# Optimization experiments

Hardware: AMD Instinct MI355X
Metric: run time of the kernel (lower is better)

Reference implementation:

```python
import jax, jax.numpy as jnp
import numpy as np

B, S, E, H, FF = 4, 2048, 512, 8, 2048
DH = E // H
EPS = 1e-6


def setup_inputs() -> dict:
    key = jax.random.key(0)
    ks = jax.random.split(key, 16)
    sc = lambda fan_in: 1.0 / np.sqrt(fan_in)
    inp = {
        "x": jax.random.normal(ks[0], (B, S, E), dtype=jnp.float32),
        "src_mask": jnp.ones((B, 1, 1, S), dtype=jnp.int32),
        # attention projections, stored [in, out]
        "wq": jax.random.uniform(ks[1], (E, E), minval=-sc(E), maxval=sc(E)),
        "bq": jnp.zeros((E,), jnp.float32),
        "wk": jax.random.uniform(ks[2], (E, E), minval=-sc(E), maxval=sc(E)),
        "bk": jnp.zeros((E,), jnp.float32),
        "wv": jax.random.uniform(ks[3], (E, E), minval=-sc(E), maxval=sc(E)),
        "bv": jnp.zeros((E,), jnp.float32),
        "wo": jax.random.uniform(ks[4], (E, E), minval=-sc(E), maxval=sc(E)),
        "bo": jnp.zeros((E,), jnp.float32),
        # feed-forward
        "w1": jax.random.uniform(ks[5], (E, FF), minval=-sc(E), maxval=sc(E)),
        "b1": jnp.zeros((FF,), jnp.float32),
        "w2": jax.random.uniform(ks[6], (FF, E), minval=-sc(FF), maxval=sc(FF)),
        "b2": jnp.zeros((E,), jnp.float32),
        # addNormLayer scalar params (alpha init 1, bias init 0)
        "alpha1": jnp.ones((1,), jnp.float32),
        "beta1": jnp.zeros((1,), jnp.float32),
        "alpha2": jnp.ones((1,), jnp.float32),
        "beta2": jnp.zeros((1,), jnp.float32),
    }
    return inp


def _norm(x, alpha, beta):
    # matches torch: mean + unbiased std (ddof=1), eps added to std
    mean = jnp.mean(x, axis=-1, keepdims=True)
    std = jnp.std(x, axis=-1, keepdims=True, ddof=1)
    return alpha * (x - mean) / (std + EPS) + beta


def reference(x, src_mask, wq, bq, wk, bk, wv, bv, wo, bo,
              w1, b1, w2, b2, alpha1, beta1, alpha2, beta2):
    # --- residual 1: pre-norm self-attention ---
    n = _norm(x, alpha1, beta1)  # [B,S,E]
    q = (n @ wq + bq).reshape(B, S, H, DH).transpose(0, 2, 1, 3)  # [B,H,S,DH]
    k = (n @ wk + bk).reshape(B, S, H, DH).transpose(0, 2, 1, 3)
    v = (n @ wv + bv).reshape(B, S, H, DH).transpose(0, 2, 1, 3)
    scores = jnp.einsum('bhqd,bhkd->bhqk', q, k) / np.sqrt(DH)  # [B,H,S,S]
    scores = jnp.where(src_mask == 0, -1e9, scores)
    attn = jax.nn.softmax(scores, axis=-1)
    ctx = jnp.einsum('bhqk,bhkd->bhqd', attn, v)  # [B,H,S,DH]
    ctx = ctx.transpose(0, 2, 1, 3).reshape(B, S, E)
    x = x + (ctx @ wo + bo)
    # --- residual 2: pre-norm FFN ---
    n2 = _norm(x, alpha2, beta2)
    ff = jax.nn.relu(n2 @ w1 + b1) @ w2 + b2
    return x + ff
```

## Files before the change

### kernel.cpp

```cpp
#include <hip/hip_runtime.h>

typedef __bf16 bfrag __attribute__((ext_vector_type(8)));
typedef float f32x4 __attribute__((ext_vector_type(4)));
typedef float f32x16 __attribute__((ext_vector_type(16)));
typedef unsigned short us8 __attribute__((ext_vector_type(8)));
typedef unsigned int u32x2 __attribute__((ext_vector_type(2)));
typedef unsigned int u32x4 __attribute__((ext_vector_type(4)));

__device__ __forceinline__ float bf2f(unsigned short s) {
  unsigned u = ((unsigned)s) << 16;
  float f;
  __builtin_memcpy(&f, &u, 4);
  return f;
}
__device__ __forceinline__ unsigned short f2bf(float f) {
  unsigned u;
  __builtin_memcpy(&u, &f, 4);
  u += 0x7fffu + ((u >> 16) & 1u);
  return (unsigned short)(u >> 16);
}
__device__ __forceinline__ float rdf(const void* p, size_t i, int isf) {
  return isf ? ((const float*)p)[i] : bf2f(((const unsigned short*)p)[i]);
}
__device__ __forceinline__ void gld16(const unsigned short* g, unsigned short* l) {
  __builtin_amdgcn_global_load_lds(
      (const __attribute__((address_space(1))) unsigned int*)g,
      (__attribute__((address_space(3))) unsigned int*)l, 16, 0, 0);
}
__device__ __forceinline__ unsigned cvtpk_bf16(float a, float b) {
  unsigned d;
  asm("v_cvt_pk_bf16_f32 %0, %1, %2" : "=v"(d) : "v"(a), "v"(b));
  return d;
}

template <int XMODE>
__device__ void norm_unit(const void* xin, const void* alpha, const void* beta,
                          unsigned short* out, int isf, int u) {
  constexpr int E = 512;
  int xf = XMODE ? 1 : isf;
  int tid = threadIdx.x;
  int wave = tid >> 6, lane = tid & 63;
  size_t tok = (size_t)u * 4 + wave;
  float v[8];
  if (xf) {
    const float* xp = (const float*)xin + tok * E + lane * 8;
    float4 a0 = *(const float4*)xp;
    float4 a1 = *(const float4*)(xp + 4);
    v[0] = a0.x; v[1] = a0.y; v[2] = a0.z; v[3] = a0.w;
    v[4] = a1.x; v[5] = a1.y; v[6] = a1.z; v[7] = a1.w;
  } else {
    us8 uu = *(const us8*)((const unsigned short*)xin + tok * E + lane * 8);
#pragma unroll
    for (int j = 0; j < 8; j++) v[j] = bf2f(uu[j]);
  }
  float s = 0.f, sq = 0.f;
#pragma unroll
  for (int j = 0; j < 8; j++) { s += v[j]; sq += v[j] * v[j]; }
#pragma unroll
  for (int off = 1; off < 64; off <<= 1) {
    s += __shfl_xor(s, off, 64);
    sq += __shfl_xor(sq, off, 64);
  }
  float mean = s * (1.0f / 512.0f);
  float var = fmaxf((sq - 512.0f * mean * mean) * (1.0f / 511.0f), 0.0f);
  float inv = rdf(alpha, 0, isf) / (sqrtf(var) + 1e-6f);
  float be = rdf(beta, 0, isf);
  us8 ov;
#pragma unroll
  for (int j = 0; j < 8; j++) ov[j] = f2bf((v[j] - mean) * inv + be);
  *(us8*)(out + tok * E + lane * 8) = ov;
}

__global__ __launch_bounds__(256) void setup_k(
    const unsigned short* __restrict__ x16,
    const void* wq, const void* wk, const void* wv, const void* wo,
    const void* w1, const void* w2,
    unsigned short* wqkvT, unsigned short* woT,
    unsigned short* w1T, unsigned short* w2T,
    const void* bq, const void* bk, const void* bv, const void* bo,
    const void* b1, const void* b2, float* __restrict__ bcat,
    const void* alpha1, const void* beta1, unsigned short* __restrict__ n1,
    int* __restrict__ flag) {
  __shared__ unsigned short tile[32][33];
  __shared__ int s_cnt;
  int tid = threadIdx.x;
  int bid = blockIdx.x;
  if (tid == 0) s_cnt = 0;
  __syncthreads();
  {
    int c = 0;
    for (int i = tid; i < 4096; i += 256) {
      unsigned short s = x16[2 * i];
      int e = (s >> 7) & 0xFF;
      if (e > 0xC2 || (e != 0 && e < 0x3D)) c++;
    }
    atomicAdd(&s_cnt, c);
  }
  __syncthreads();
  const int isf = (s_cnt > 256) ? 1 : 0;
  if (bid == 0 && tid == 0) flag[0] = isf;

  if (bid >= 3090) {
    norm_unit<0>(x16, alpha1, beta1, n1, isf, bid - 3090);
    return;
  }
  if (bid >= 3072) {
    int i = (bid - 3072) * 256 + tid;
    if (i < 4608) {
      float v;
      if (i < 512) v = rdf(bq, i, isf);
      else if (i < 1024) v = rdf(bk, i - 512, isf);
      else if (i < 1536) v = rdf(bv, i - 1024, isf);
      else if (i < 2048) v = rdf(bo, i - 1536, isf);
      else if (i < 4096) v = rdf(b1, i - 2048, isf);
      else v = rdf(b2, i - 4096, isf);
      bcat[i] = v;
    }
    return;
  }
  const void* W;
  unsigned short* Wt;
  int K, N, t;
  if (bid < 1024) {
    K = 512; N = 512; t = bid & 255;
    if (bid < 256) { W = wq; Wt = wqkvT; }
    else if (bid < 512) { W = wk; Wt = wqkvT + 262144; }
    else if (bid < 768) { W = wv; Wt = wqkvT + 524288; }
    else { W = wo; Wt = woT; }
  } else if (bid < 2048) {
    W = w1; Wt = w1T; K = 512; N = 2048; t = bid - 1024;
  } else {
    W = w2; Wt = w2T; K = 2048; N = 512; t = bid - 2048;
  }
  int nx = N >> 5;
  int n0 = (t % nx) * 32, k0 = (t / nx) * 32;
#pragma unroll
  for (int i = 0; i < 4; i++) {
    int e = tid + i * 256;
    int r = e >> 5, c = e & 31;
    tile[r][c] = f2bf(rdf(W, (size_t)(k0 + r) * N + n0 + c, isf));
  }
  __syncthreads();
#pragma unroll
  for (int i = 0; i < 4; i++) {
    int e = tid + i * 256;
    int r = e >> 5, c = e & 31;
    Wt[(size_t)(n0 + r) * K + k0 + c] = tile[c][r];
  }
}

__global__ __launch_bounds__(256) void vtrans_k(
    const unsigned short* __restrict__ qkb, unsigned short* __restrict__ vbt) {
  __shared__ unsigned short tile[32][33];
  int tid = threadIdx.x;
  int u = blockIdx.x;
  int s0 = (u & 63) * 32;
  int d0 = ((u >> 6) & 1) * 32;
  int bh = u >> 7, b = bh >> 3, h = bh & 7;
#pragma unroll
  for (int i = 0; i < 4; i++) {
    int e = tid + i * 256;
    int r = e >> 5, c = e & 31;
    tile[r][c] = qkb[((size_t)b * 2048 + s0 + r) * 1536 + 1024 + h * 64 + d0 + c];
  }
  __syncthreads();
#pragma unroll
  for (int i = 0; i < 4; i++) {
    int e = tid + i * 256;
    int r = e >> 5, c = e & 31;
    vbt[((size_t)bh * 64 + d0 + r) * 2048 + s0 + c] = tile[c][r];
  }
}

__global__ __launch_bounds__(256) void norm2_k(
    const void* __restrict__ xin, const void* __restrict__ alpha,
    const void* __restrict__ beta, unsigned short* __restrict__ out,
    const int* __restrict__ flag) {
  norm_unit<1>(xin, alpha, beta, out, flag[0], blockIdx.x);
}

template <int TN, int RES, int OUTM, int RELU>
__global__ __launch_bounds__(256, 3) void gemm2_k(
    const unsigned short* __restrict__ A,
    const unsigned short* __restrict__ Bt,
    const float* __restrict__ bias,
    const void* __restrict__ res,
    void* __restrict__ outp,
    int N, int K, const int* __restrict__ flag) {
  constexpr int MT = (TN == 128) ? 4 : 2;
  constexpr int BROWS = TN / 4;
  __shared__ alignas(16) unsigned short As[128 * 64];
  __shared__ alignas(16) unsigned short Bs[TN * 64];
  int isf = flag[0];
  int outf32 = (OUTM == 1) || (OUTM == 2 && isf);
  int tid = threadIdx.x;
  int wave = tid >> 6, lane = tid & 63;
  int quad = lane >> 4, l16 = lane & 15, l7 = l16 & 7;
  int wm = (TN == 128) ? (wave >> 1) : wave;
  int wn = (TN == 128) ? (wave & 1) : 0;
  size_t m0 = (size_t)blockIdx.x * 128;
  size_t n0 = (size_t)blockIdx.y * TN;

  int lrow = lane >> 3;
  int gcol = 8 * ((lane & 7) ^ lrow);

  const unsigned short* ag = A + (m0 + wave * 32 + lrow) * K + gcol;
  const unsigned short* bg = Bt + (n0 + wave * BROWS + lrow) * K + gcol;
  unsigned short* asl = &As[(wave * 32) * 64];
  unsigned short* bsl = &Bs[(wave * BROWS) * 64];

  f32x4 acc[MT][4];
#pragma unroll
  for (int i = 0; i < MT; i++)
#pragma unroll
    for (int j = 0; j < 4; j++) acc[i][j] = {0.f, 0.f, 0.f, 0.f};

  for (int k0 = 0; k0 < K; k0 += 64) {
    __syncthreads();
#pragma unroll
    for (int c = 0; c < 4; c++)
      gld16(ag + (size_t)(8 * c) * K + k0, asl + (8 * c) * 64);
#pragma unroll
    for (int c = 0; c < BROWS / 8; c++)
      gld16(bg + (size_t)(8 * c) * K + k0, bsl + (8 * c) * 64);
    __syncthreads();
#pragma unroll
    for (int ko = 0; ko < 2; ko++) {
      int slot = ((4 * ko + quad) ^ l7) * 8;
      bfrag af[MT], bf[4];
#pragma unroll
      for (int i = 0; i < MT; i++)
        af[i] = *(const bfrag*)&As[(wm * (MT * 16) + i * 16 + l16) * 64 + slot];
#pragma unroll
      for (int j = 0; j < 4; j++)
        bf[j] = *(const bfrag*)&Bs[(wn * 64 + j * 16 + l16) * 64 + slot];
#pragma unroll
      for (int i = 0; i < MT; i++)
#pragma unroll
        for (int j = 0; j < 4; j++)
          acc[i][j] = __builtin_amdgcn_mfma_f32_16x16x32_bf16(af[i], bf[j], acc[i][j], 0, 0, 0);
    }
  }
#pragma unroll
  for (int j = 0; j < 4; j++) {
    size_t n = n0 + wn * 64 + j * 16 + l16;
    float bv = bias[n];
#pragma unroll
    for (int i = 0; i < MT; i++) {
#pragma unroll
      for (int r = 0; r < 4; r++) {
        size_t m = m0 + wm * (MT * 16) + i * 16 + quad * 4 + r;
        float vv = acc[i][j][r] + bv;
        if (RELU) vv = fmaxf(vv, 0.0f);
        if (RES == 1) vv += rdf(res, m * N + n, isf);
        else if (RES == 2) vv += ((const float*)res)[m * N + n];
        if (outf32) ((float*)outp)[m * N + n] = vv;
        else ((unsigned short*)outp)[m * N + n] = f2bf(vv);
      }
    }
  }
}

__global__ __launch_bounds__(256, 2) void attn_k(
    const unsigned short* __restrict__ qkb,
    const unsigned short* __restrict__ vbt,
    const int* __restrict__ mask,
    unsigned short* __restrict__ ctx) {
  constexpr int S = 2048;
  __shared__ alignas(16) unsigned short Kt[64 * 64];
  __shared__ alignas(16) unsigned short Vt[64 * 64];
  __shared__ alignas(16) float mskf[64];
  __shared__ float linv[128];
  int tid = threadIdx.x, wave = tid >> 6, lane = tid & 63;
  int l32 = lane & 31, hi = lane >> 5;
  int q0 = blockIdx.x * 128;
  int bh = blockIdx.y, b = bh >> 3, h = bh & 7;
  size_t rowbase = (size_t)b * S;
  const float SC = 0.18033688f;

  bfrag qf[4];
  {
    const unsigned short* qp =
        qkb + (rowbase + q0 + wave * 32 + l32) * 1536 + h * 64 + hi * 8;
#pragma unroll
    for (int ds = 0; ds < 4; ds++) qf[ds] = *(const bfrag*)(qp + ds * 16);
  }

  int srow_l = lane >> 3;
  int sc = lane & 7;
  const unsigned short* kgb = qkb + 512 + h * 64;
  const unsigned short* vgb = vbt + (size_t)bh * 64 * S;

  f32x16 o[2];
#pragma unroll
  for (int i = 0; i < 16; i++) { o[0][i] = 0.f; o[1][i] = 0.f; }
  float l_i = 0.f;

  for (int kt = 0; kt < S; kt += 64) {
    __syncthreads();
    {
#pragma unroll
      for (int i = 0; i < 2; i++) {
        int r = wave * 16 + i * 8 + srow_l;
        gld16(kgb + (rowbase + kt + r) * 1536 + (size_t)((sc ^ (r & 7)) * 8),
              &Kt[(wave * 16 + i * 8) * 64]);
        gld16(vgb + (size_t)r * S + kt + (size_t)((sc ^ (r & 7)) * 8),
              &Vt[(wave * 16 + i * 8) * 64]);
      }
    }
    if (tid < 64) mskf[tid] = mask[rowbase + kt + tid] ? 0.0f : -1e5f;
    __syncthreads();

    f32x16 pacc[2];
#pragma unroll
    for (int t = 0; t < 2; t++)
#pragma unroll
      for (int i = 0; i < 16; i++) pacc[t][i] = 0.f;
#pragma unroll
    for (int t = 0; t < 2; t++) {
      int r = t * 32 + l32;
#pragma unroll
      for (int ds = 0; ds < 4; ds++) {
        int phys = ((2 * ds + hi) ^ (r & 7)) * 8;
        bfrag kf = *(const bfrag*)&Kt[r * 64 + phys];
        pacc[t] = __builtin_amdgcn_mfma_f32_32x32x16_bf16(kf, qf[ds], pacc[t], 0, 0, 0);
      }
    }

    unsigned pb[2][8];
#pragma unroll
    for (int t = 0; t < 2; t++) {
#pragma unroll
      for (int g = 0; g < 4; g++) {
        float4 m4 = *(const float4*)&mskf[t * 32 + g * 8 + hi * 4];
        float p0 = __builtin_amdgcn_exp2f(fminf(fmaf(pacc[t][g * 4 + 0], SC, m4.x), 50.0f));
        float p1 = __builtin_amdgcn_exp2f(fminf(fmaf(pacc[t][g * 4 + 1], SC, m4.y), 50.0f));
        float p2 = __builtin_amdgcn_exp2f(fminf(fmaf(pacc[t][g * 4 + 2], SC, m4.z), 50.0f));
        float p3 = __builtin_amdgcn_exp2f(fminf(fmaf(pacc[t][g * 4 + 3], SC, m4.w), 50.0f));
        l_i += (p0 + p1) + (p2 + p3);
        pb[t][g * 2] = cvtpk_bf16(p0, p1);
        pb[t][g * 2 + 1] = cvtpk_bf16(p2, p3);
      }
    }

#pragma unroll
    for (int ks = 0; ks < 4; ks++) {
      int t = ks >> 1, e = ks & 1;
      u32x2 sA = __builtin_amdgcn_permlane32_swap(pb[t][4 * e + 0], pb[t][4 * e + 2], false, false);
      u32x2 sB = __builtin_amdgcn_permlane32_swap(pb[t][4 * e + 1], pb[t][4 * e + 3], false, false);
      u32x4 pw = {sA.x, sB.x, sA.y, sB.y};
      bfrag pf = __builtin_bit_cast(bfrag, pw);
#pragma unroll
      for (int dt = 0; dt < 2; dt++) {
        int r = dt * 32 + l32;
        int phys = ((2 * ks + hi) ^ (r & 7)) * 8;
        bfrag vf = *(const bfrag*)&Vt[r * 64 + phys];
        o[dt] = __builtin_amdgcn_mfma_f32_32x32x16_bf16(pf, vf, o[dt], 0, 0, 0);
      }
    }
  }

  {
    unsigned lu = __builtin_bit_cast(unsigned, l_i);
    u32x2 lr = __builtin_amdgcn_permlane32_swap(lu, lu, false, false);
    float l_tot = __builtin_bit_cast(float, lr.x) + __builtin_bit_cast(float, lr.y);
    if (lane < 32) linv[wave * 32 + l32] = 1.0f / fmaxf(l_tot, 1e-30f);
  }
  __syncthreads();
#pragma unroll
  for (int dt = 0; dt < 2; dt++) {
#pragma unroll
    for (int reg = 0; reg < 16; reg++) {
      int ql = (reg & 3) + 8 * (reg >> 2) + 4 * hi;
      size_t qrow = rowbase + q0 + wave * 32 + ql;
      ctx[qrow * 512 + h * 64 + dt * 32 + l32] =
          f2bf(o[dt][reg] * linv[wave * 32 + ql]);
    }
  }
}

extern "C" void kernel_launch(void* const* d_in, const int* in_sizes, int n_in,
                              void* d_out, int out_size, void* d_ws, size_t ws_size,
                              hipStream_t stream) {
  const unsigned short* x = (const unsigned short*)d_in[0];
  const int* mask         = (const int*)d_in[1];
  const void* wq = d_in[2];  const void* bq = d_in[3];
  const void* wk = d_in[4];  const void* bk = d_in[5];
  const void* wv = d_in[6];  const void* bv = d_in[7];
  const void* wo = d_in[8];  const void* bo = d_in[9];
  const void* w1 = d_in[10]; const void* b1 = d_in[11];
  const void* w2 = d_in[12]; const void* b2 = d_in[13];
  const void* alpha1 = d_in[14]; const void* beta1 = d_in[15];
  const void* alpha2 = d_in[16]; const void* beta2 = d_in[17];

  char* ws = (char*)d_ws;
  int* flag            = (int*)(ws + 0);
  unsigned short* wqkvT= (unsigned short*)(ws + 65536);
  unsigned short* woT  = (unsigned short*)(ws + 1638400);
  unsigned short* w1T  = (unsigned short*)(ws + 2162688);
  unsigned short* w2T  = (unsigned short*)(ws + 4259840);
  float*          bcat = (float*)         (ws + 6356992);
  float*          x1   = (float*)         (ws + 6422528);
  unsigned short* n1   = (unsigned short*)(ws + 23199744);
  unsigned short* qkb  = (unsigned short*)(ws + 31588352);
  unsigned short* vbt  = (unsigned short*)(ws + 56754176);
  unsigned short* ff1  = qkb;

  dim3 blk(256);

  setup_k<<<5138, blk, 0, stream>>>(x, wq, wk, wv, wo, w1, w2,
                                    wqkvT, woT, w1T, w2T,
                                    bq, bk, bv, bo, b1, b2, bcat,
                                    alpha1, beta1, n1, flag);
  gemm2_k<128, 0, 0, 0><<<dim3(64, 12), blk, 0, stream>>>(n1, wqkvT, bcat, nullptr, qkb, 1536, 512, flag);
  vtrans_k<<<4096, blk, 0, stream>>>(qkb, vbt);
  attn_k<<<dim3(16, 32), blk, 0, stream>>>(qkb, vbt, mask, n1);
  gemm2_k<64, 1, 1, 0><<<dim3(64, 8), blk, 0, stream>>>(n1, woT, bcat + 1536, (const void*)x, x1, 512, 512, flag);
  norm2_k<<<2048, blk, 0, stream>>>(x1, alpha2, beta2, n1, flag);
  gemm2_k<128, 0, 0, 1><<<dim3(64, 16), blk, 0, stream>>>(n1, w1T, bcat + 2048, nullptr, ff1, 2048, 512, flag);
  gemm2_k<64, 2, 2, 0><<<dim3(64, 8), blk, 0, stream>>>(ff1, w2T, bcat + 4096, x1, d_out, 512, 2048, flag);
}
```

Before: 286.2 us.

## Double-buffer K/V tiles in attention, preload mask, remap blocks for locality

The attention kernel now keeps two LDS buffers for K and V. It prefetches the next 64-key tile while computing on the current one, using one barrier per iteration instead of two. The whole key mask row is converted into LDS once at kernel start rather than per tile. The launch becomes a 1D grid whose block index is permuted so that the query blocks of one (batch, head) are spread across blocks spaced 8 apart, likely to improve K/V cache sharing across XCDs. LDS use grows to about 40KB per block, which could limit occupancy.

```diff
diff --git a/kernel.cpp b/kernel.cpp
--- a/kernel.cpp
+++ b/kernel.cpp
@@ -267,14 +267,18 @@
     const int* __restrict__ mask,
     unsigned short* __restrict__ ctx) {
   constexpr int S = 2048;
-  __shared__ alignas(16) unsigned short Kt[64 * 64];
-  __shared__ alignas(16) unsigned short Vt[64 * 64];
-  __shared__ alignas(16) float mskf[64];
+  __shared__ alignas(16) unsigned short Kt[2][64 * 64];
+  __shared__ alignas(16) unsigned short Vt[2][64 * 64];
+  __shared__ alignas(16) float mskf[S];
   __shared__ float linv[128];
   int tid = threadIdx.x, wave = tid >> 6, lane = tid & 63;
   int l32 = lane & 31, hi = lane >> 5;
-  int q0 = blockIdx.x * 128;
-  int bh = blockIdx.y, b = bh >> 3, h = bh & 7;
+
+  int lin = blockIdx.x;
+  int work = (lin & 7) * 64 + (lin >> 3);
+  int bh = work >> 4;
+  int q0 = (work & 15) * 128;
+  int b = bh >> 3, h = bh & 7;
   size_t rowbase = (size_t)b * S;
   const float SC = 0.18033688f;
 
@@ -291,25 +295,30 @@
   const unsigned short* kgb = qkb + 512 + h * 64;
   const unsigned short* vgb = vbt + (size_t)bh * 64 * S;
 
+  auto STAGE = [&](int buf, int kt) {
+#pragma unroll
+    for (int i = 0; i < 2; i++) {
+      int r = wave * 16 + i * 8 + srow_l;
+      gld16(kgb + (rowbase + kt + r) * 1536 + (size_t)((sc ^ (r & 7)) * 8),
+            &Kt[buf][(wave * 16 + i * 8) * 64]);
+      gld16(vgb + (size_t)r * S + kt + (size_t)((sc ^ (r & 7)) * 8),
+            &Vt[buf][(wave * 16 + i * 8) * 64]);
+    }
+  };
+
   f32x16 o[2];
 #pragma unroll
   for (int i = 0; i < 16; i++) { o[0][i] = 0.f; o[1][i] = 0.f; }
   float l_i = 0.f;
 
-  for (int kt = 0; kt < S; kt += 64) {
-    __syncthreads();
-    {
-#pragma unroll
-      for (int i = 0; i < 2; i++) {
-        int r = wave * 16 + i * 8 + srow_l;
-        gld16(kgb + (rowbase + kt + r) * 1536 + (size_t)((sc ^ (r & 7)) * 8),
-              &Kt[(wave * 16 + i * 8) * 64]);
-        gld16(vgb + (size_t)r * S + kt + (size_t)((sc ^ (r & 7)) * 8),
-              &Vt[(wave * 16 + i * 8) * 64]);
-      }
-    }
-    if (tid < 64) mskf[tid] = mask[rowbase + kt + tid] ? 0.0f : -1e5f;
-    __syncthreads();
+  STAGE(0, 0);
+  for (int i = tid; i < S; i += 256) mskf[i] = mask[rowbase + i] ? 0.0f : -1e5f;
+  __syncthreads();
+
+  for (int it = 0; it < S / 64; it++) {
+    int kt = it * 64;
+    int cur = it & 1;
+    if (it + 1 < S / 64) STAGE(cur ^ 1, kt + 64);
 
     f32x16 pacc[2];
 #pragma unroll
@@ -322,7 +331,7 @@
 #pragma unroll
       for (int ds = 0; ds < 4; ds++) {
         int phys = ((2 * ds + hi) ^ (r & 7)) * 8;
-        bfrag kf = *(const bfrag*)&Kt[r * 64 + phys];
+        bfrag kf = *(const bfrag*)&Kt[cur][r * 64 + phys];
         pacc[t] = __builtin_amdgcn_mfma_f32_32x32x16_bf16(kf, qf[ds], pacc[t], 0, 0, 0);
       }
     }
@@ -332,7 +341,7 @@
     for (int t = 0; t < 2; t++) {
 #pragma unroll
       for (int g = 0; g < 4; g++) {
-        float4 m4 = *(const float4*)&mskf[t * 32 + g * 8 + hi * 4];
+        float4 m4 = *(const float4*)&mskf[kt + t * 32 + g * 8 + hi * 4];
         float p0 = __builtin_amdgcn_exp2f(fminf(fmaf(pacc[t][g * 4 + 0], SC, m4.x), 50.0f));
         float p1 = __builtin_amdgcn_exp2f(fminf(fmaf(pacc[t][g * 4 + 1], SC, m4.y), 50.0f));
         float p2 = __builtin_amdgcn_exp2f(fminf(fmaf(pacc[t][g * 4 + 2], SC, m4.z), 50.0f));
@@ -354,10 +363,11 @@
       for (int dt = 0; dt < 2; dt++) {
         int r = dt * 32 + l32;
         int phys = ((2 * ks + hi) ^ (r & 7)) * 8;
-        bfrag vf = *(const bfrag*)&Vt[r * 64 + phys];
+        bfrag vf = *(const bfrag*)&Vt[cur][r * 64 + phys];
         o[dt] = __builtin_amdgcn_mfma_f32_32x32x16_bf16(pf, vf, o[dt], 0, 0, 0);
       }
     }
+    __syncthreads();
   }
 
   {
@@ -414,7 +424,7 @@
                                     alpha1, beta1, n1, flag);
   gemm2_k<128, 0, 0, 0><<<dim3(64, 12), blk, 0, stream>>>(n1, wqkvT, bcat, nullptr, qkb, 1536, 512, flag);
   vtrans_k<<<4096, blk, 0, stream>>>(qkb, vbt);
-  attn_k<<<dim3(16, 32), blk, 0, stream>>>(qkb, vbt, mask, n1);
+  attn_k<<<512, blk, 0, stream>>>(qkb, vbt, mask, n1);
   gemm2_k<64, 1, 1, 0><<<dim3(64, 8), blk, 0, stream>>>(n1, woT, bcat + 1536, (const void*)x, x1, 512, 512, flag);
   norm2_k<<<2048, blk, 0, stream>>>(x1, alpha2, beta2, n1, flag);
   gemm2_k<128, 0, 0, 1><<<dim3(64, 16), blk, 0, stream>>>(n1, w1T, bcat + 2048, nullptr, ff1, 2048, 512, flag);
```

Measured after the change: 284.7 us. Within noise of the previous version (-0.5%).
